# Performance work log

Hardware: AMD Instinct MI355X
Metric: run time of the kernel (lower is better)

Reference implementation:

```python
import jax, jax.numpy as jnp
import numpy as np

B, L, D, H, NL = 16, 256, 768, 12, 4
HD = D // H          # head size = 64; also edge-feature embedding dim
V, E, C, F = 30000, 50, 2, 3072
CLS_ID = 1


def _pos_emb(length, dim):
    # standard sinusoidal positional embedding [L, D]
    pos = jnp.arange(length, dtype=jnp.float32)[:, None]
    div = jnp.exp(-np.log(10000.0) * jnp.arange(0, dim, 2, dtype=jnp.float32) / dim)
    ang = pos * div[None, :]
    pe = jnp.zeros((length, dim), jnp.float32)
    return pe.at[:, 0::2].set(jnp.sin(ang)).at[:, 1::2].set(jnp.cos(ang))


def _ln(x, g, b, eps=1e-5):
    m = x.mean(-1, keepdims=True)
    v = x.var(-1, keepdims=True)
    return (x - m) * jax.lax.rsqrt(v + eps) * g + b


def setup_inputs() -> dict:
    key = jax.random.key(0)
    ks = jax.random.split(key, 16)
    s = 0.02
    word_ids = jax.random.randint(ks[0], (B, L), 0, V).at[:, 0].set(CLS_ID)
    batched_adj = jax.random.bernoulli(ks[1], 0.3, (B, L, L)) | jnp.eye(L, dtype=bool)[None]
    edge_types = jax.random.randint(ks[2], (B, L, L), 0, E)
    word_emb = (jax.random.normal(ks[3], (V, D)) * s).at[0].set(0.0)   # padding_idx=0
    edge_emb = (jax.random.normal(ks[4], (E, HD)) * s).at[0].set(0.0)  # padding_idx=0
    pw = lambda k, shp: jax.random.normal(k, shp) * s
    return {
        "word_ids": word_ids, "batched_adj": batched_adj, "edge_types": edge_types,
        "word_emb": word_emb, "edge_emb": edge_emb,
        "Wq": pw(ks[5], (NL, D, D)), "bq": jnp.zeros((NL, D)),
        "Wk": pw(ks[6], (NL, D, D)), "bk": jnp.zeros((NL, D)),
        "Wv": pw(ks[7], (NL, D, D)), "bv": jnp.zeros((NL, D)),
        "Wo": pw(ks[8], (NL, D, D)), "bo": jnp.zeros((NL, D)),
        "ln1_g": jnp.ones((NL, D)), "ln1_b": jnp.zeros((NL, D)),
        "W1": pw(ks[9], (NL, D, F)), "b1": jnp.zeros((NL, F)),
        "W2": pw(ks[10], (NL, F, D)), "b2": jnp.zeros((NL, D)),
        "ln2_g": jnp.ones((NL, D)), "ln2_b": jnp.zeros((NL, D)),
        "cls_W": pw(ks[11], (D, C)), "cls_b": jnp.zeros((C,)),
    }


def reference(word_ids, batched_adj, edge_types, word_emb, edge_emb,
              Wq, bq, Wk, bk, Wv, bv, Wo, bo, ln1_g, ln1_b,
              W1, b1, W2, b2, ln2_g, ln2_b, cls_W, cls_b):
    # node features: word embedding + positional embedding
    h = word_emb[word_ids] + _pos_emb(L, D)[None]          # [B,L,D]
    scale = 1.0 / np.sqrt(HD)
    eemb = edge_emb[edge_types]                             # [B,L,L,HD] edge key features
    neg = jnp.asarray(-1e9, h.dtype)
    mask = batched_adj[:, None]                             # [B,1,L,L]
    for l in range(NL):
        q = (h @ Wq[l] + bq[l]).reshape(B, L, H, HD)
        k = (h @ Wk[l] + bk[l]).reshape(B, L, H, HD)
        v = (h @ Wv[l] + bv[l]).reshape(B, L, H, HD)
        # scores: node-node + query . edge-key-feature, adjacency-masked
        scores = jnp.einsum('bihd,bjhd->bhij', q, k)
        scores = scores + jnp.einsum('bihd,bijd->bhij', q, eemb)
        scores = jnp.where(mask, scores * scale, neg)
        att = jax.nn.softmax(scores, axis=-1)               # [B,H,L,L]
        out = jnp.einsum('bhij,bjhd->bihd', att, v).reshape(B, L, D)
        h = _ln(h + (out @ Wo[l] + bo[l]), ln1_g[l], ln1_b[l])
        ff = jax.nn.relu(h @ W1[l] + b1[l]) @ W2[l] + b2[l]
        h = _ln(h + ff, ln2_g[l], ln2_b[l])
    cls_h = h[:, 0]                                         # CLS pooling
    logits = cls_h @ cls_W + cls_b                          # [B,C]
    return logits
```

## Files before the change

kernel.cpp:

```cpp
#include <hip/hip_runtime.h>
#include <hip/hip_bf16.h>

#define BB 16
#define LL 256
#define DD 768
#define HH 12
#define HDD 64
#define NLL 4
#define FF 3072
#define EE 50

typedef unsigned short ushort_t;
typedef __bf16 bf16x8 __attribute__((ext_vector_type(8)));
typedef float f32x4 __attribute__((ext_vector_type(4)));

__device__ __forceinline__ float b2f(ushort_t u) {
    union { unsigned int i; float f; } x; x.i = ((unsigned int)u) << 16; return x.f;
}
__device__ __forceinline__ ushort_t f2b(float f) {
    unsigned int u = __builtin_bit_cast(unsigned int, f);
    unsigned int r = u + 0x7fffu + ((u >> 16) & 1u);
    return (ushort_t)(r >> 16);
}

__device__ __forceinline__ void gl2lds16(const void* g, void* l) {
    __builtin_amdgcn_global_load_lds(
        (const __attribute__((address_space(1))) unsigned int*)g,
        (__attribute__((address_space(3))) unsigned int*)l,
        16, 0, 0);
}

__global__ __launch_bounds__(256) void transpose_f2b(
    const float* __restrict__ in, ushort_t* __restrict__ out, int R, int C)
{
    __shared__ ushort_t tile[32][33];
    int c0 = blockIdx.x * 32, r0 = blockIdx.y * 32;
    int tx = threadIdx.x, ty = threadIdx.y;
#pragma unroll
    for (int i = 0; i < 32; i += 8)
        tile[ty + i][tx] = f2b(in[(long)(r0 + ty + i) * C + c0 + tx]);
    __syncthreads();
#pragma unroll
    for (int i = 0; i < 32; i += 8)
        out[(long)(c0 + ty + i) * R + r0 + tx] = tile[tx][ty + i];
}

__global__ __launch_bounds__(256) void embed_kernel(
    const int* __restrict__ wids, const float* __restrict__ wemb,
    float* __restrict__ hf, ushort_t* __restrict__ hb)
{
    long idx = (long)blockIdx.x * 256 + threadIdx.x;
    int d = (int)(idx % DD);
    int t = (int)(idx / DD);
    int lpos = t & (LL - 1);
    int wid = wids[t];
    float freq = expf(-9.210340371976184f * (float)(d & ~1) * (1.f / (float)DD));
    float ang = (float)lpos * freq;
    float pe = (d & 1) ? cosf(ang) : sinf(ang);
    float hv = wemb[(long)wid * DD + d] + pe;
    hf[idx] = hv;
    hb[idx] = f2b(hv);
}

__global__ __launch_bounds__(256) void gemm_bf16(
    const ushort_t* __restrict__ A, const ushort_t* __restrict__ Bt,
    const float* __restrict__ bias,
    ushort_t* __restrict__ outb, float* __restrict__ outf,
    int M, int N, int K, int relu)
{
    __shared__ __align__(16) ushort_t As[128 * 32];
    __shared__ __align__(16) ushort_t Bs[128 * 32];
    const int tid = threadIdx.x;
    const int wave = tid >> 6, lane = tid & 63;
    const int quad = lane >> 4, l16 = lane & 15;
    const int m0 = blockIdx.y * 128, n0 = blockIdx.x * 128;
    const int wm = (wave >> 1) * 64, wn = (wave & 1) * 64;
    const ushort_t* Ab = A + (long)m0 * K;
    const ushort_t* Bb = Bt + (long)n0 * K;

    f32x4 acc[4][4];
#pragma unroll
    for (int mi = 0; mi < 4; ++mi)
#pragma unroll
        for (int ni = 0; ni < 4; ++ni) acc[mi][ni] = (f32x4){0.f, 0.f, 0.f, 0.f};

    const int nk = K >> 5;
    for (int kt = 0; kt < nk; ++kt) {
        const int k0 = kt << 5;
        __syncthreads();
#pragma unroll
        for (int i = 0; i < 2; ++i) {
            int c = tid + i * 256;
            int row = c >> 2, kc = (c & 3) * 8;
            char* la = (char*)As + (wave * 1024 + i * 4096);
            char* lb = (char*)Bs + (wave * 1024 + i * 4096);
            gl2lds16(&Ab[(long)row * K + k0 + kc], la);
            gl2lds16(&Bb[(long)row * K + k0 + kc], lb);
        }
        __syncthreads();
        bf16x8 af[4], bfr[4];
#pragma unroll
        for (int t = 0; t < 4; ++t)
            af[t] = *(const bf16x8*)&As[(wm + t * 16 + l16) * 32 + quad * 8];
#pragma unroll
        for (int t = 0; t < 4; ++t)
            bfr[t] = *(const bf16x8*)&Bs[(wn + t * 16 + l16) * 32 + quad * 8];
#pragma unroll
        for (int mi = 0; mi < 4; ++mi)
#pragma unroll
            for (int ni = 0; ni < 4; ++ni)
                acc[mi][ni] = __builtin_amdgcn_mfma_f32_16x16x32_bf16(
                    af[mi], bfr[ni], acc[mi][ni], 0, 0, 0);
    }

#pragma unroll
    for (int ni = 0; ni < 4; ++ni) {
        int col = n0 + wn + ni * 16 + l16;
        float bv = bias ? bias[col] : 0.f;
#pragma unroll
        for (int mi = 0; mi < 4; ++mi) {
#pragma unroll
            for (int r = 0; r < 4; ++r) {
                int row = m0 + wm + mi * 16 + quad * 4 + r;
                float vv = acc[mi][ni][r] + bv;
                if (relu) vv = fmaxf(vv, 0.f);
                if (outb) outb[(long)row * N + col] = f2b(vv);
                if (outf) outf[(long)row * N + col] = vv;
            }
        }
    }
}

#define QS_STR 72
#define VT_STR 264
#define P_STR  264
#define S_STR  257
#define PE_STR 53

__global__ __launch_bounds__(256) void attn_kernel(
    const ushort_t* __restrict__ q, const ushort_t* __restrict__ k,
    const ushort_t* __restrict__ v,
    const int* __restrict__ adjm, const int* __restrict__ etyp,
    const float* __restrict__ eemb, ushort_t* __restrict__ out)
{
    __shared__ __align__(16) char smem[64448];
    ushort_t* VT = (ushort_t*)smem;
    float*    S  = (float*)(smem + 33792);
    ushort_t* P  = (ushort_t*)(smem + 50240);
    float*    Pe = (float*)(smem + 58688);
    char*     U  = smem + 62080;
    float* invrow = (float*)(smem + 64384);
    ushort_t* Qs = (ushort_t*)U;
    float*    red = (float*)U;

    const int blk = blockIdx.x;
    const int qt = blk & 15;
    const int h  = (blk >> 4) % HH;
    const int b  = blk / (16 * HH);
    const int i0 = qt * 16;
    const int tid = threadIdx.x;
    const int wave = tid >> 6, lane = tid & 63;
    const int quad = lane >> 4, l16 = lane & 15;

    if (tid < 128) {
        int row = tid >> 3, d0 = (tid & 7) * 8;
        *(int4*)&Qs[row * QS_STR + d0] =
            *(const int4*)&q[((long)(b * LL + i0 + row)) * DD + h * HDD + d0];
    }
#pragma unroll
    for (int i = 0; i < 8; ++i) {
        int c = tid + i * 256;
        int j = c >> 3, d0 = (c & 7) * 8;
        int4 raw = *(const int4*)&v[((long)(b * LL + j)) * DD + h * HDD + d0];
        const ushort_t* vals = (const ushort_t*)&raw;
#pragma unroll
        for (int u = 0; u < 8; ++u) VT[(d0 + u) * VT_STR + j] = vals[u];
    }
    __syncthreads();

    {
        int e = wave * 16 + l16;
        f32x4 acc = (f32x4){0.f, 0.f, 0.f, 0.f};
#pragma unroll
        for (int kk = 0; kk < 2; ++kk) {
            bf16x8 af = *(const bf16x8*)&Qs[l16 * QS_STR + kk * 32 + quad * 8];
            bf16x8 bf = (bf16x8){0, 0, 0, 0, 0, 0, 0, 0};
            if (e < EE) {
                const float* ep = &eemb[(long)e * HDD + kk * 32 + quad * 8];
#pragma unroll
                for (int u = 0; u < 8; ++u) bf[u] = (__bf16)ep[u];
            }
            acc = __builtin_amdgcn_mfma_f32_16x16x32_bf16(af, bf, acc, 0, 0, 0);
        }
        if (e < EE) {
#pragma unroll
            for (int r = 0; r < 4; ++r) Pe[(quad * 4 + r) * PE_STR + e] = acc[r];
        }
    }

#pragma unroll
    for (int jt = 0; jt < 4; ++jt) {
        int jtile = wave * 4 + jt;
        int j = jtile * 16 + l16;
        f32x4 acc = (f32x4){0.f, 0.f, 0.f, 0.f};
#pragma unroll
        for (int kk = 0; kk < 2; ++kk) {
            bf16x8 af = *(const bf16x8*)&Qs[l16 * QS_STR + kk * 32 + quad * 8];
            bf16x8 bf = *(const bf16x8*)&k[((long)(b * LL + j)) * DD + h * HDD + kk * 32 + quad * 8];
            acc = __builtin_amdgcn_mfma_f32_16x16x32_bf16(af, bf, acc, 0, 0, 0);
        }
#pragma unroll
        for (int r = 0; r < 4; ++r)
            S[(quad * 4 + r) * S_STR + jtile * 16 + l16] = acc[r];
    }
    __syncthreads();

    {
        const int row = tid & 15, seg = tid >> 4;
        const int i = i0 + row;
        const int* etp = etyp + ((long)(b * LL + i)) * LL + seg * 16;
        const int* adp = adjm + ((long)(b * LL + i)) * LL + seg * 16;
        int etv[16], adv[16];
#pragma unroll
        for (int t = 0; t < 4; ++t) {
            *(int4*)&etv[t * 4] = *(const int4*)&etp[t * 4];
            *(int4*)&adv[t * 4] = *(const int4*)&adp[t * 4];
        }
        float vals[16];
        float pmax = -1e30f;
#pragma unroll
        for (int c = 0; c < 16; ++c) {
            float s = S[row * S_STR + seg * 16 + c];
            float pe = Pe[row * PE_STR + etv[c]];
            float vv = adv[c] ? (s + pe) * 0.125f : -1e30f;
            vals[c] = vv;
            pmax = fmaxf(pmax, vv);
        }
        red[row * 17 + seg] = pmax;
        __syncthreads();
        float m = -1e30f;
#pragma unroll
        for (int g = 0; g < 16; ++g) m = fmaxf(m, red[row * 17 + g]);
        float sum = 0.f;
#pragma unroll
        for (int c = 0; c < 16; ++c) {
            float p = __expf(vals[c] - m);
            ushort_t pb = f2b(p);
            sum += b2f(pb);
            P[row * P_STR + seg * 16 + c] = pb;
        }
        red[272 + row * 17 + seg] = sum;
        __syncthreads();
        if (tid < 16) {
            float tot = 0.f;
#pragma unroll
            for (int g = 0; g < 16; ++g) tot += red[272 + tid * 17 + g];
            invrow[tid] = 1.f / tot;
        }
        __syncthreads();
    }

    {
        f32x4 acc = (f32x4){0.f, 0.f, 0.f, 0.f};
#pragma unroll
        for (int kt = 0; kt < 8; ++kt) {
            bf16x8 af = *(const bf16x8*)&P[l16 * P_STR + kt * 32 + quad * 8];
            bf16x8 bf = *(const bf16x8*)&VT[(wave * 16 + l16) * VT_STR + kt * 32 + quad * 8];
            acc = __builtin_amdgcn_mfma_f32_16x16x32_bf16(af, bf, acc, 0, 0, 0);
        }
#pragma unroll
        for (int r = 0; r < 4; ++r) {
            int row = quad * 4 + r;
            float ov = acc[r] * invrow[row];
            out[((long)(b * LL + i0 + row)) * DD + h * HDD + wave * 16 + l16] = f2b(ov);
        }
    }
}

__global__ __launch_bounds__(256) void ln_kernel(
    float* __restrict__ hf, ushort_t* __restrict__ hb,
    const float* __restrict__ proj,
    const float* __restrict__ g, const float* __restrict__ be)
{
    const int r = blockIdx.x, tid = threadIdx.x;
    const long rb = (long)r * DD;
    float x[3];
#pragma unroll
    for (int i = 0; i < 3; ++i) { int d = tid + i * 256; x[i] = hf[rb + d] + proj[rb + d]; }
    float s = x[0] + x[1] + x[2];
    float s2 = x[0] * x[0] + x[1] * x[1] + x[2] * x[2];
#pragma unroll
    for (int o = 1; o < 64; o <<= 1) { s += __shfl_xor(s, o); s2 += __shfl_xor(s2, o); }
    __shared__ float rs[4], rq[4];
    int wave = tid >> 6;
    if ((tid & 63) == 0) { rs[wave] = s; rq[wave] = s2; }
    __syncthreads();
    float S  = rs[0] + rs[1] + rs[2] + rs[3];
    float S2 = rq[0] + rq[1] + rq[2] + rq[3];
    float mean = S * (1.f / (float)DD);
    float var  = S2 * (1.f / (float)DD) - mean * mean;
    float rstd = rsqrtf(var + 1e-5f);
#pragma unroll
    for (int i = 0; i < 3; ++i) {
        int d = tid + i * 256;
        float y = (x[i] - mean) * rstd * g[d] + be[d];
        hf[rb + d] = y;
        hb[rb + d] = f2b(y);
    }
}

__global__ __launch_bounds__(256) void cls_kernel(
    const float* __restrict__ hf, const float* __restrict__ W,
    const float* __restrict__ bias, float* __restrict__ out)
{
    int b = blockIdx.x, tid = threadIdx.x;
    const float* hr = hf + (long)b * LL * DD;
    float p0 = 0.f, p1 = 0.f;
    for (int d = tid; d < DD; d += 256) {
        float hv = hr[d];
        p0 = fmaf(hv, W[d * 2 + 0], p0);
        p1 = fmaf(hv, W[d * 2 + 1], p1);
    }
#pragma unroll
    for (int o = 1; o < 64; o <<= 1) { p0 += __shfl_xor(p0, o); p1 += __shfl_xor(p1, o); }
    __shared__ float r0[4], r1[4];
    int wave = tid >> 6;
    if ((tid & 63) == 0) { r0[wave] = p0; r1[wave] = p1; }
    __syncthreads();
    if (tid == 0) {
        out[b * 2 + 0] = r0[0] + r0[1] + r0[2] + r0[3] + bias[0];
        out[b * 2 + 1] = r1[0] + r1[1] + r1[2] + r1[3] + bias[1];
    }
}

extern "C" void kernel_launch(void* const* d_in, const int* in_sizes, int n_in,
                              void* d_out, int out_size, void* d_ws, size_t ws_size,
                              hipStream_t stream)
{
    const int* word_ids = (const int*)d_in[0];
    const int* adjm     = (const int*)d_in[1];
    const int* etyp     = (const int*)d_in[2];
    const float* wemb   = (const float*)d_in[3];
    const float* eemb   = (const float*)d_in[4];
    const float* Wq     = (const float*)d_in[5];
    const float* bq     = (const float*)d_in[6];
    const float* Wk     = (const float*)d_in[7];
    const float* bk     = (const float*)d_in[8];
    const float* Wv     = (const float*)d_in[9];
    const float* bv     = (const float*)d_in[10];
    const float* Wo     = (const float*)d_in[11];
    const float* bo     = (const float*)d_in[12];
    const float* ln1g   = (const float*)d_in[13];
    const float* ln1b   = (const float*)d_in[14];
    const float* W1     = (const float*)d_in[15];
    const float* b1     = (const float*)d_in[16];
    const float* W2     = (const float*)d_in[17];
    const float* b2     = (const float*)d_in[18];
    const float* ln2g   = (const float*)d_in[19];
    const float* ln2b   = (const float*)d_in[20];
    const float* clsW   = (const float*)d_in[21];
    const float* clsb   = (const float*)d_in[22];
    float* outp = (float*)d_out;

    char* ws = (char*)d_ws;
    size_t off = 0;
    auto alloc = [&](size_t bytes) -> char* {
        char* p = ws + off;
        off += (bytes + 255) & ~(size_t)255;
        return p;
    };
    const size_t DxD = (size_t)DD * DD;
    const size_t DxF = (size_t)DD * FF;
    const size_t TOK = (size_t)BB * LL;

    float*    hf  = (float*)alloc(TOK * DD * 4);
    ushort_t* hb  = (ushort_t*)alloc(TOK * DD * 2);
    ushort_t* tw  = (ushort_t*)alloc(DxF * 2);
    ushort_t* qb  = (ushort_t*)alloc(TOK * DD * 2);
    ushort_t* kb2 = (ushort_t*)alloc(TOK * DD * 2);
    ushort_t* vb2 = (ushort_t*)alloc(TOK * DD * 2);
    ushort_t* ao  = (ushort_t*)alloc(TOK * DD * 2);
    float*    pjf = (float*)alloc(TOK * DD * 4);
    ushort_t* ff1 = qb;
    (void)ws_size; (void)in_sizes; (void)n_in; (void)out_size;

    embed_kernel<<<(int)(TOK * DD / 256), 256, 0, stream>>>(word_ids, wemb, hf, hb);

    dim3 tb(32, 8, 1);
    const int M = (int)TOK;
    for (int l = 0; l < NLL; ++l) {
        transpose_f2b<<<dim3(24, 24), tb, 0, stream>>>(Wq + (size_t)l * DxD, tw, DD, DD);
        gemm_bf16<<<dim3(DD / 128, M / 128), 256, 0, stream>>>(
            hb, tw, bq + l * DD, qb, nullptr, M, DD, DD, 0);
        transpose_f2b<<<dim3(24, 24), tb, 0, stream>>>(Wk + (size_t)l * DxD, tw, DD, DD);
        gemm_bf16<<<dim3(DD / 128, M / 128), 256, 0, stream>>>(
            hb, tw, bk + l * DD, kb2, nullptr, M, DD, DD, 0);
        transpose_f2b<<<dim3(24, 24), tb, 0, stream>>>(Wv + (size_t)l * DxD, tw, DD, DD);
        gemm_bf16<<<dim3(DD / 128, M / 128), 256, 0, stream>>>(
            hb, tw, bv + l * DD, vb2, nullptr, M, DD, DD, 0);
        attn_kernel<<<BB * HH * 16, 256, 0, stream>>>(qb, kb2, vb2, adjm, etyp, eemb, ao);
        transpose_f2b<<<dim3(24, 24), tb, 0, stream>>>(Wo + (size_t)l * DxD, tw, DD, DD);
        gemm_bf16<<<dim3(DD / 128, M / 128), 256, 0, stream>>>(
            ao, tw, bo + l * DD, nullptr, pjf, M, DD, DD, 0);
        ln_kernel<<<M, 256, 0, stream>>>(hf, hb, pjf, ln1g + l * DD, ln1b + l * DD);
        transpose_f2b<<<dim3(96, 24), tb, 0, stream>>>(W1 + (size_t)l * DxF, tw, DD, FF);
        gemm_bf16<<<dim3(FF / 128, M / 128), 256, 0, stream>>>(
            hb, tw, b1 + l * FF, ff1, nullptr, M, FF, DD, 1);
        transpose_f2b<<<dim3(24, 96), tb, 0, stream>>>(W2 + (size_t)l * DxF, tw, FF, DD);
        gemm_bf16<<<dim3(DD / 128, M / 128), 256, 0, stream>>>(
            ff1, tw, b2 + l * DD, nullptr, pjf, M, DD, FF, 0);
        ln_kernel<<<M, 256, 0, stream>>>(hf, hb, pjf, ln2g + l * DD, ln2b + l * DD);
    }
    cls_kernel<<<BB, 256, 0, stream>>>(hf, clsW, clsb, outp);
}
```

Before: 1.390 ms.

## Fuse QKV GEMM, add split-K for narrow GEMMs, pretranspose all weights upfront

Fuses the Q, K and V projections into one GEMM with N=2304 writing an interleaved qkv buffer, with a small kernel that builds the concatenated bias. Adds split-K over blockIdx.z for the output projection and FFN2 GEMMs, which have only 192 tiles, to fill more CUs; the LayerNorm kernel sums the partial outputs. When the workspace is large enough, all layer weights are transposed to bf16 in a few batched launches before the layer loop. The costs are extra partial-sum traffic in fp32 and larger workspace use.

```diff
diff --git a/kernel.cpp b/kernel.cpp
--- a/kernel.cpp
+++ b/kernel.cpp
@@ -9,6 +9,8 @@
 #define NLL 4
 #define FF 3072
 #define EE 50
+#define QKVS 2304
+#define TOKD ((size_t)BB * LL * DD)
 
 typedef unsigned short ushort_t;
 typedef __bf16 bf16x8 __attribute__((ext_vector_type(8)));
@@ -31,9 +33,12 @@
 }
 
 __global__ __launch_bounds__(256) void transpose_f2b(
-    const float* __restrict__ in, ushort_t* __restrict__ out, int R, int C)
+    const float* __restrict__ in, ushort_t* __restrict__ out, int R, int C,
+    long inZ, long outZ)
 {
     __shared__ ushort_t tile[32][33];
+    in  += (long)blockIdx.z * inZ;
+    out += (long)blockIdx.z * outZ;
     int c0 = blockIdx.x * 32, r0 = blockIdx.y * 32;
     int tx = threadIdx.x, ty = threadIdx.y;
 #pragma unroll
@@ -43,6 +48,18 @@
 #pragma unroll
     for (int i = 0; i < 32; i += 8)
         out[(long)(c0 + ty + i) * R + r0 + tx] = tile[tx][ty + i];
+}
+
+__global__ __launch_bounds__(256) void fuse_bias_kernel(
+    const float* __restrict__ bq, const float* __restrict__ bk,
+    const float* __restrict__ bv, int l, float* __restrict__ out)
+{
+    int n = blockIdx.x * 256 + threadIdx.x;
+    if (n >= QKVS) return;
+    float v = (n < DD) ? bq[l * DD + n]
+            : (n < 2 * DD) ? bk[l * DD + n - DD]
+            : bv[l * DD + n - 2 * DD];
+    out[n] = v;
 }
 
 __global__ __launch_bounds__(256) void embed_kernel(
@@ -66,7 +83,7 @@
     const ushort_t* __restrict__ A, const ushort_t* __restrict__ Bt,
     const float* __restrict__ bias,
     ushort_t* __restrict__ outb, float* __restrict__ outf,
-    int M, int N, int K, int relu)
+    int M, int N, int K, int Ksl, int relu)
 {
     __shared__ __align__(16) ushort_t As[128 * 32];
     __shared__ __align__(16) ushort_t Bs[128 * 32];
@@ -74,6 +91,8 @@
     const int wave = tid >> 6, lane = tid & 63;
     const int quad = lane >> 4, l16 = lane & 15;
     const int m0 = blockIdx.y * 128, n0 = blockIdx.x * 128;
+    const int z = blockIdx.z;
+    const int kbase = z * Ksl;
     const int wm = (wave >> 1) * 64, wn = (wave & 1) * 64;
     const ushort_t* Ab = A + (long)m0 * K;
     const ushort_t* Bb = Bt + (long)n0 * K;
@@ -84,9 +103,9 @@
 #pragma unroll
         for (int ni = 0; ni < 4; ++ni) acc[mi][ni] = (f32x4){0.f, 0.f, 0.f, 0.f};
 
-    const int nk = K >> 5;
+    const int nk = Ksl >> 5;
     for (int kt = 0; kt < nk; ++kt) {
-        const int k0 = kt << 5;
+        const int k0 = kbase + (kt << 5);
         __syncthreads();
 #pragma unroll
         for (int i = 0; i < 2; ++i) {
@@ -113,10 +132,11 @@
                     af[mi], bfr[ni], acc[mi][ni], 0, 0, 0);
     }
 
+    float* outfz = outf ? outf + (size_t)z * M * N : nullptr;
 #pragma unroll
     for (int ni = 0; ni < 4; ++ni) {
         int col = n0 + wn + ni * 16 + l16;
-        float bv = bias ? bias[col] : 0.f;
+        float bv = (bias && z == 0) ? bias[col] : 0.f;
 #pragma unroll
         for (int mi = 0; mi < 4; ++mi) {
 #pragma unroll
@@ -125,7 +145,7 @@
                 float vv = acc[mi][ni][r] + bv;
                 if (relu) vv = fmaxf(vv, 0.f);
                 if (outb) outb[(long)row * N + col] = f2b(vv);
-                if (outf) outf[(long)row * N + col] = vv;
+                if (outfz) outfz[(long)row * N + col] = vv;
             }
         }
     }
@@ -138,8 +158,7 @@
 #define PE_STR 53
 
 __global__ __launch_bounds__(256) void attn_kernel(
-    const ushort_t* __restrict__ q, const ushort_t* __restrict__ k,
-    const ushort_t* __restrict__ v,
+    const ushort_t* __restrict__ qkv,
     const int* __restrict__ adjm, const int* __restrict__ etyp,
     const float* __restrict__ eemb, ushort_t* __restrict__ out)
 {
@@ -165,13 +184,13 @@
     if (tid < 128) {
         int row = tid >> 3, d0 = (tid & 7) * 8;
         *(int4*)&Qs[row * QS_STR + d0] =
-            *(const int4*)&q[((long)(b * LL + i0 + row)) * DD + h * HDD + d0];
+            *(const int4*)&qkv[((long)(b * LL + i0 + row)) * QKVS + h * HDD + d0];
     }
 #pragma unroll
     for (int i = 0; i < 8; ++i) {
         int c = tid + i * 256;
         int j = c >> 3, d0 = (c & 7) * 8;
-        int4 raw = *(const int4*)&v[((long)(b * LL + j)) * DD + h * HDD + d0];
+        int4 raw = *(const int4*)&qkv[((long)(b * LL + j)) * QKVS + 2 * DD + h * HDD + d0];
         const ushort_t* vals = (const ushort_t*)&raw;
 #pragma unroll
         for (int u = 0; u < 8; ++u) VT[(d0 + u) * VT_STR + j] = vals[u];
@@ -206,7 +225,7 @@
 #pragma unroll
         for (int kk = 0; kk < 2; ++kk) {
             bf16x8 af = *(const bf16x8*)&Qs[l16 * QS_STR + kk * 32 + quad * 8];
-            bf16x8 bf = *(const bf16x8*)&k[((long)(b * LL + j)) * DD + h * HDD + kk * 32 + quad * 8];
+            bf16x8 bf = *(const bf16x8*)&qkv[((long)(b * LL + j)) * QKVS + DD + h * HDD + kk * 32 + quad * 8];
             acc = __builtin_amdgcn_mfma_f32_16x16x32_bf16(af, bf, acc, 0, 0, 0);
         }
 #pragma unroll
@@ -279,14 +298,19 @@
 
 __global__ __launch_bounds__(256) void ln_kernel(
     float* __restrict__ hf, ushort_t* __restrict__ hb,
-    const float* __restrict__ proj,
+    const float* __restrict__ proj, int nparts,
     const float* __restrict__ g, const float* __restrict__ be)
 {
     const int r = blockIdx.x, tid = threadIdx.x;
     const long rb = (long)r * DD;
     float x[3];
 #pragma unroll
-    for (int i = 0; i < 3; ++i) { int d = tid + i * 256; x[i] = hf[rb + d] + proj[rb + d]; }
+    for (int i = 0; i < 3; ++i) {
+        int d = tid + i * 256;
+        float t = hf[rb + d];
+        for (int p = 0; p < nparts; ++p) t += proj[(size_t)p * TOKD + rb + d];
+        x[i] = t;
+    }
     float s = x[0] + x[1] + x[2];
     float s2 = x[0] * x[0] + x[1] * x[1] + x[2] * x[2];
 #pragma unroll
@@ -372,44 +396,70 @@
     const size_t DxD = (size_t)DD * DD;
     const size_t DxF = (size_t)DD * FF;
     const size_t TOK = (size_t)BB * LL;
+    const size_t LSTR = (size_t)QKVS * DD + DxD + 2 * DxF;
 
     float*    hf  = (float*)alloc(TOK * DD * 4);
     ushort_t* hb  = (ushort_t*)alloc(TOK * DD * 2);
-    ushort_t* tw  = (ushort_t*)alloc(DxF * 2);
-    ushort_t* qb  = (ushort_t*)alloc(TOK * DD * 2);
-    ushort_t* kb2 = (ushort_t*)alloc(TOK * DD * 2);
-    ushort_t* vb2 = (ushort_t*)alloc(TOK * DD * 2);
+    ushort_t* qkv = (ushort_t*)alloc(TOK * QKVS * 2);
     ushort_t* ao  = (ushort_t*)alloc(TOK * DD * 2);
     float*    pjf = (float*)alloc(TOK * DD * 4);
-    ushort_t* ff1 = qb;
-    (void)ws_size; (void)in_sizes; (void)n_in; (void)out_size;
+    ushort_t* tw  = (ushort_t*)alloc(DxF * 2);
+    ushort_t* ff1 = qkv;
+    size_t tier1 = off + TOK * DD * 4;
+    size_t tier2 = tier1 + 2 * TOK * DD * 4;
+    size_t tier3 = tier2 + NLL * LSTR * 2;
+    int S_o = 1, S_f = 1;
+    ushort_t* cache = nullptr;
+    if (ws_size >= tier1) { (void)alloc(TOK * DD * 4); S_o = 2; S_f = 2; }
+    if (ws_size >= tier2) { (void)alloc(2 * TOK * DD * 4); S_f = 4; }
+    if (ws_size >= tier3) { cache = (ushort_t*)alloc(NLL * LSTR * 2); }
+    (void)in_sizes; (void)n_in; (void)out_size;
+
+    dim3 tb(32, 8, 1);
+    if (cache) {
+        transpose_f2b<<<dim3(24, 24, NLL), tb, 0, stream>>>(Wq, cache,                 DD, DD, DxD, LSTR);
+        transpose_f2b<<<dim3(24, 24, NLL), tb, 0, stream>>>(Wk, cache + DD * DD,       DD, DD, DxD, LSTR);
+        transpose_f2b<<<dim3(24, 24, NLL), tb, 0, stream>>>(Wv, cache + 2 * DD * DD,   DD, DD, DxD, LSTR);
+        transpose_f2b<<<dim3(24, 24, NLL), tb, 0, stream>>>(Wo, cache + 3 * DD * DD,   DD, DD, DxD, LSTR);
+        transpose_f2b<<<dim3(96, 24, NLL), tb, 0, stream>>>(W1, cache + 4 * DD * DD,   DD, FF, DxF, LSTR);
+        transpose_f2b<<<dim3(24, 96, NLL), tb, 0, stream>>>(W2, cache + 4 * DD * DD + DxF, FF, DD, DxF, LSTR);
+    }
 
     embed_kernel<<<(int)(TOK * DD / 256), 256, 0, stream>>>(word_ids, wemb, hf, hb);
 
-    dim3 tb(32, 8, 1);
     const int M = (int)TOK;
     for (int l = 0; l < NLL; ++l) {
-        transpose_f2b<<<dim3(24, 24), tb, 0, stream>>>(Wq + (size_t)l * DxD, tw, DD, DD);
-        gemm_bf16<<<dim3(DD / 128, M / 128), 256, 0, stream>>>(
-            hb, tw, bq + l * DD, qb, nullptr, M, DD, DD, 0);
-        transpose_f2b<<<dim3(24, 24), tb, 0, stream>>>(Wk + (size_t)l * DxD, tw, DD, DD);
-        gemm_bf16<<<dim3(DD / 128, M / 128), 256, 0, stream>>>(
-            hb, tw, bk + l * DD, kb2, nullptr, M, DD, DD, 0);
-        transpose_f2b<<<dim3(24, 24), tb, 0, stream>>>(Wv + (size_t)l * DxD, tw, DD, DD);
-        gemm_bf16<<<dim3(DD / 128, M / 128), 256, 0, stream>>>(
-            hb, tw, bv + l * DD, vb2, nullptr, M, DD, DD, 0);
-        attn_kernel<<<BB * HH * 16, 256, 0, stream>>>(qb, kb2, vb2, adjm, etyp, eemb, ao);
-        transpose_f2b<<<dim3(24, 24), tb, 0, stream>>>(Wo + (size_t)l * DxD, tw, DD, DD);
-        gemm_bf16<<<dim3(DD / 128, M / 128), 256, 0, stream>>>(
-            ao, tw, bo + l * DD, nullptr, pjf, M, DD, DD, 0);
-        ln_kernel<<<M, 256, 0, stream>>>(hf, hb, pjf, ln1g + l * DD, ln1b + l * DD);
-        transpose_f2b<<<dim3(96, 24), tb, 0, stream>>>(W1 + (size_t)l * DxF, tw, DD, FF);
-        gemm_bf16<<<dim3(FF / 128, M / 128), 256, 0, stream>>>(
-            hb, tw, b1 + l * FF, ff1, nullptr, M, FF, DD, 1);
-        transpose_f2b<<<dim3(24, 96), tb, 0, stream>>>(W2 + (size_t)l * DxF, tw, FF, DD);
-        gemm_bf16<<<dim3(DD / 128, M / 128), 256, 0, stream>>>(
-            ff1, tw, b2 + l * DD, nullptr, pjf, M, DD, FF, 0);
-        ln_kernel<<<M, 256, 0, stream>>>(hf, hb, pjf, ln2g + l * DD, ln2b + l * DD);
+        const ushort_t *BtQKV, *BtO, *BtW1, *BtW2;
+        if (cache) {
+            const ushort_t* base = cache + (size_t)l * LSTR;
+            BtQKV = base; BtO = base + 3 * DD * DD;
+            BtW1 = base + 4 * DD * DD; BtW2 = base + 4 * DD * DD + DxF;
+        } else {
+            BtQKV = tw; BtO = tw; BtW1 = tw; BtW2 = tw;
+        }
+        fuse_bias_kernel<<<9, 256, 0, stream>>>(bq, bk, bv, l, pjf);
+        if (!cache) {
+            transpose_f2b<<<dim3(24, 24), tb, 0, stream>>>(Wq + (size_t)l * DxD, tw,               DD, DD, 0, 0);
+            transpose_f2b<<<dim3(24, 24), tb, 0, stream>>>(Wk + (size_t)l * DxD, tw + DD * DD,     DD, DD, 0, 0);
+            transpose_f2b<<<dim3(24, 24), tb, 0, stream>>>(Wv + (size_t)l * DxD, tw + 2 * DD * DD, DD, DD, 0, 0);
+        }
+        gemm_bf16<<<dim3(QKVS / 128, M / 128, 1), 256, 0, stream>>>(
+            hb, BtQKV, pjf, qkv, nullptr, M, QKVS, DD, DD, 0);
+        attn_kernel<<<BB * HH * 16, 256, 0, stream>>>(qkv, adjm, etyp, eemb, ao);
+        if (!cache)
+            transpose_f2b<<<dim3(24, 24), tb, 0, stream>>>(Wo + (size_t)l * DxD, tw, DD, DD, 0, 0);
+        gemm_bf16<<<dim3(DD / 128, M / 128, S_o), 256, 0, stream>>>(
+            ao, BtO, bo + l * DD, nullptr, pjf, M, DD, DD, DD / S_o, 0);
+        ln_kernel<<<M, 256, 0, stream>>>(hf, hb, pjf, S_o, ln1g + l * DD, ln1b + l * DD);
+        if (!cache)
+            transpose_f2b<<<dim3(96, 24), tb, 0, stream>>>(W1 + (size_t)l * DxF, tw, DD, FF, 0, 0);
+        gemm_bf16<<<dim3(FF / 128, M / 128, 1), 256, 0, stream>>>(
+            hb, BtW1, b1 + l * FF, ff1, nullptr, M, FF, DD, DD, 1);
+        if (!cache)
+            transpose_f2b<<<dim3(24, 96), tb, 0, stream>>>(W2 + (size_t)l * DxF, tw, FF, DD, 0, 0);
+        gemm_bf16<<<dim3(DD / 128, M / 128, S_f), 256, 0, stream>>>(
+            ff1, BtW2, b2 + l * DD, nullptr, pjf, M, DD, FF, FF / S_f, 0);
+        ln_kernel<<<M, 256, 0, stream>>>(hf, hb, pjf, S_f, ln2g + l * DD, ln2b + l * DD);
     }
     cls_kernel<<<BB, 256, 0, stream>>>(hf, clsW, clsb, outp);
 }
```

Measured after the change: 1.248 ms. 1.11x faster.
